# Optimization experiments

Hardware: AMD Instinct MI355X
Metric: run time of the kernel (lower is better)

The kernel has to match this reference:

```python
import jax, jax.numpy as jnp
import numpy as np

K = 5            # Chebyshev order (hard-coded in ManEmbedder conv_kwargs)
LAMBDA_MAX = 3.0 # fixed lambda_max from init
N_NODES = 100000
N_EDGES = 400000
N_GRAPHS = 64
H1, H2 = 128, 512


def _seg_sum(vals, idx, n):
    return jax.ops.segment_sum(vals, idx, num_segments=n)


def _cheb_edge_weights(edge_index, n_nodes):
    """Scaled Laplacian L_hat = 2*(I - D^-1/2 A D^-1/2)/lambda_max - I as edge weights.
    Matches PyG get_laplacian('sym') + ChebConv.__norm__ with fixed lambda_max.
    Degrees are computed at row = edge_index[0] (as in get_laplacian)."""
    row, col = edge_index[0], edge_index[1]
    ones = jnp.ones(row.shape[0], jnp.float32)
    deg = _seg_sum(ones, row, n_nodes)
    dinv = jnp.where(deg > 0, jax.lax.rsqrt(jnp.maximum(deg, 1e-12)), 0.0)
    w_edge = -(dinv[row] * dinv[col]) * (2.0 / LAMBDA_MAX)  # off-diagonal of L_hat
    w_loop = 2.0 / LAMBDA_MAX - 1.0                          # diagonal of L_hat (scalar)
    return w_edge, w_loop


def cheb_conv(x, edge_index, W, b, reverse):
    """PyG ChebConv. flow='target_to_source' (reverse=False): aggregate at row, gather at col.
    reverse=True flips the propagation direction (source_to_target)."""
    n = x.shape[0]
    w_edge, w_loop = _cheb_edge_weights(edge_index, n)
    row, col = edge_index[0], edge_index[1]
    src, dst = (row, col) if reverse else (col, row)

    def prop(h):  # L_hat @ h via gather-scale-scatter + diagonal term
        return _seg_sum(w_edge[:, None] * h[src], dst, n) + w_loop * h

    tx0 = x
    out = tx0 @ W[0]
    tx1 = prop(tx0)
    out = out + tx1 @ W[1]
    for k in range(2, K):
        tx2 = 2.0 * prop(tx1) - tx0
        out = out + tx2 @ W[k]
        tx0, tx1 = tx1, tx2
    return out + b


def bidir_block(x, edge_index, Wf, bf, Wb, bb):
    # Bidirectional: one ChebConv per edge direction, outputs summed.
    return cheb_conv(x, edge_index, Wf, bf, False) + cheb_conv(x, edge_index, Wb, bb, True)


def setup_inputs() -> dict:
    key = jax.random.key(0)
    ks = jax.random.split(key, 12)
    x = jax.random.normal(ks[0], (N_NODES, 1), jnp.float32)
    edge_index = jax.random.randint(ks[1], (2, N_EDGES), 0, N_NODES, dtype=jnp.int64)
    batch = jnp.sort(jax.random.randint(ks[2], (N_NODES,), 0, N_GRAPHS, dtype=jnp.int64))

    def glorot(k, shape):
        fan_in, fan_out = shape[-2], shape[-1]
        s = (6.0 / (fan_in + fan_out)) ** 0.5
        return jax.random.uniform(k, shape, jnp.float32, -s, s)

    return {
        "x": x, "edge_index": edge_index, "batch": batch,
        "W1f": glorot(ks[3], (K, 1, H1)),  "b1f": jnp.zeros((H1,), jnp.float32),
        "W1b": glorot(ks[4], (K, 1, H1)),  "b1b": jnp.zeros((H1,), jnp.float32),
        "W2f": glorot(ks[5], (K, H1, H2)), "b2f": jnp.zeros((H2,), jnp.float32),
        "W2b": glorot(ks[6], (K, H1, H2)), "b2b": jnp.zeros((H2,), jnp.float32),
    }


def reference(x, edge_index, batch, W1f, b1f, W1b, b1b, W2f, b2f, W2b, b2b):
    h = jax.nn.relu(bidir_block(x, edge_index, W1f, b1f, W1b, b1b))
    h = jax.nn.relu(bidir_block(h, edge_index, W2f, b2f, W2b, b2b))
    # global mean pool over batch index -> [N_GRAPHS, 512]
    summed = _seg_sum(h, batch, N_GRAPHS)
    counts = _seg_sum(jnp.ones((h.shape[0],), jnp.float32), batch, N_GRAPHS)
    return summed / jnp.maximum(counts, 1.0)[:, None]
```

## Files before the change

kernel.cpp:

```cpp
#include <hip/hip_runtime.h>
#include <hip/hip_bf16.h>

typedef unsigned short u16;
typedef unsigned int u32;
typedef __attribute__((ext_vector_type(4))) float f32x4;
typedef __attribute__((ext_vector_type(8))) short bf16x8;

struct __align__(8) ew_t { int s; float w; };

#define WLOOP (2.0f/3.0f - 1.0f)
#define WEDGE (-(2.0f/3.0f))

__device__ __forceinline__ float bf2f(u16 h){ u32 u = ((u32)h)<<16; float f; __builtin_memcpy(&f,&u,4); return f; }
__device__ __forceinline__ u16 f2bf(float f){ u32 u; __builtin_memcpy(&u,&f,4); u32 r = u + 0x7fffu + ((u>>16)&1u); return (u16)(r>>16); }

__device__ __forceinline__ void async16(u16* lds, const u16* g){
  __builtin_amdgcn_global_load_lds((const __attribute__((address_space(1))) u32*)g,
                                   (__attribute__((address_space(3))) u32*)lds, 16, 0, 0);
}

__global__ void k_hist(const int* __restrict__ ei, int E, int* cntf, int* cntb){
  int e = blockIdx.x*256 + threadIdx.x; if (e>=E) return;
  atomicAdd(&cntf[ei[e]],1); atomicAdd(&cntb[ei[E+e]],1);
}
__global__ void k_dinv(const int* __restrict__ cntf, float* dinv, int N){
  int n = blockIdx.x*256+threadIdx.x; if(n>=N) return;
  int d = cntf[n]; dinv[n] = d>0 ? rsqrtf((float)d) : 0.f;
}
__global__ void k_scanA(const int* __restrict__ cnt, int* excl, int* bsum, int n){
  __shared__ int sh[256]; int i = blockIdx.x*256+threadIdx.x;
  int v = (i<n)? cnt[i]:0; sh[threadIdx.x]=v; __syncthreads();
  for (int off=1; off<256; off<<=1){
    int t = (threadIdx.x>=off)? sh[threadIdx.x-off]:0; __syncthreads();
    sh[threadIdx.x]+=t; __syncthreads();
  }
  if (i<n) excl[i]=sh[threadIdx.x]-v;
  if (threadIdx.x==255) bsum[blockIdx.x]=sh[255];
}
__global__ void k_scanB(int* bsum, int nb, int* total){
  __shared__ int sh[512]; int t = threadIdx.x;
  int v = (t<nb)? bsum[t]:0; sh[t]=v; __syncthreads();
  for(int off=1; off<512; off<<=1){
    int a = (t>=off)? sh[t-off]:0; __syncthreads();
    sh[t]+=a; __syncthreads();
  }
  if (t<nb) bsum[t]=sh[t]-v;
  if (t==511) *total = sh[511];
}
__global__ void k_scanC(int* excl, const int* __restrict__ bsum, int n, int* cur){
  int i = blockIdx.x*256+threadIdx.x; if(i>=n) return;
  int v = excl[i]+bsum[blockIdx.x]; excl[i]=v; cur[i]=v;
}
__global__ void k_fill(const int* __restrict__ ei, int E, const float* __restrict__ dinv,
                       int* curf, int* curb, ew_t* ewf, ew_t* ewb){
  int e = blockIdx.x*256+threadIdx.x; if(e>=E) return;
  int r = ei[e], c = ei[E+e];
  float w = WEDGE * dinv[r]*dinv[c];
  int pf = atomicAdd(&curf[r],1); ewf[pf] = {c, w};
  int pb = atomicAdd(&curb[c],1); ewb[pb] = {r, w};
}

__global__ void k_sprop(const float* __restrict__ t1f, const float* __restrict__ t0f, float* df,
                        const float* __restrict__ t1b, const float* __restrict__ t0b, float* db,
                        const int* __restrict__ offf, const ew_t* __restrict__ ewfa,
                        const int* __restrict__ offb, const ew_t* __restrict__ ewba,
                        int N){
  int i = blockIdx.x*256+threadIdx.x;
  int dir = 0; if (i >= N){ i -= N; dir = 1; }
  if (i >= N) return;
  const float* t1; const float* t0; float* d; const int* off; const ew_t* ew;
  if (dir==0){ t1=t1f; t0=t0f; d=df; off=offf; ew=ewfa; }
  else       { t1=t1b; t0=t0b; d=db; off=offb; ew=ewba; }
  float a = WLOOP * t1[i];
  int e = off[i], e1 = off[i+1];
  for (; e+4<=e1; e+=4){
    ew_t p0=ew[e], p1=ew[e+1], p2=ew[e+2], p3=ew[e+3];
    float v0=t1[p0.s], v1=t1[p1.s], v2=t1[p2.s], v3=t1[p3.s];
    a += p0.w*v0 + p1.w*v1 + p2.w*v2 + p3.w*v3;
  }
  for (; e<e1; ++e){ ew_t p=ew[e]; a += p.w*t1[p.s]; }
  d[i] = t0 ? (2.f*a - t0[i]) : a;
}

__global__ void k_expand(const float* __restrict__ x,
   const float* __restrict__ cf1, const float* __restrict__ cf2, const float* __restrict__ cf3, const float* __restrict__ cf4,
   const float* __restrict__ cb1, const float* __restrict__ cb2, const float* __restrict__ cb3, const float* __restrict__ cb4,
   const float* __restrict__ W1f, const float* __restrict__ b1f,
   const float* __restrict__ W1b, const float* __restrict__ b1b,
   u16* __restrict__ T, int N){
  __shared__ float swf[640], swb[640], sbias[128];
  int tid = threadIdx.x;
  for (int i=tid;i<640;i+=256){ swf[i]=W1f[i]; swb[i]=W1b[i]; }
  if (tid<128) sbias[tid]=b1f[tid]+b1b[tid];
  __syncthreads();
  int j = tid & 127; int n = blockIdx.x*2 + (tid>>7);
  if (n>=N) return;
  float xx = x[n];
  float acc = sbias[j] + xx*(swf[j]+swb[j]);
  acc += cf1[n]*swf[128+j]; acc += cf2[n]*swf[256+j]; acc += cf3[n]*swf[384+j]; acc += cf4[n]*swf[512+j];
  acc += cb1[n]*swb[128+j]; acc += cb2[n]*swb[256+j]; acc += cb3[n]*swb[384+j]; acc += cb4[n]*swb[512+j];
  T[(size_t)n*1152 + j] = f2bf(fmaxf(acc,0.f));
}

__global__ void k_vprop(u16* __restrict__ T,
   const int* __restrict__ offf, const ew_t* __restrict__ ewfa,
   const int* __restrict__ offb, const ew_t* __restrict__ ewba,
   int ssf, int dsf, int psf, int ssb, int dsb, int psb, int N){
  int gid = blockIdx.x*256 + threadIdx.x;
  int l = threadIdx.x & 63, li = l & 15;
  int nd = (gid>>6)*4 + (l>>4);
  int dir = 0; if (nd >= N){ nd -= N; dir = 1; }
  bool alive = nd < N;
  int wid = alive ? nd : 0;
  const int* off; const ew_t* ew; int ss,ds,ps;
  if (!dir){ off=offf;ew=ewfa;ss=ssf;ds=dsf;ps=psf; }
  else     { off=offb;ew=ewba;ss=ssb;ds=dsb;ps=psb; }

  const u16* Trow = T + (size_t)ss*128 + li*8;
  bf16x8 sv = *(const bf16x8*)(Trow + (size_t)wid*1152);
  float a[8];
  #pragma unroll
  for (int q=0;q<8;q++) a[q] = WLOOP * bf2f((u16)sv[q]);

  int e0 = alive ? off[wid]   : 0;
  int e1 = alive ? off[wid+1] : 0;
  int deg = e1 - e0;
  int dm = max(deg, __shfl_xor(deg, 16));
  dm = max(dm, __shfl_xor(dm, 32));

  for (int j=0; j<dm; j+=2){
    bool a0v = j   < deg;
    bool a1v = j+1 < deg;
    ew_t p0 = ew[e0 + (a0v ? j   : 0)];
    ew_t p1 = ew[e0 + (a1v ? j+1 : 0)];
    float w0 = a0v ? p0.w : 0.f;
    float w1 = a1v ? p1.w : 0.f;
    int s0 = a0v ? p0.s : wid;
    int s1 = a1v ? p1.s : wid;
    bf16x8 n0 = *(const bf16x8*)(Trow + (size_t)s0*1152);
    bf16x8 n1 = *(const bf16x8*)(Trow + (size_t)s1*1152);
    #pragma unroll
    for (int q=0;q<8;q++) a[q] += w0*bf2f((u16)n0[q]) + w1*bf2f((u16)n1[q]);
  }

  float r[8];
  if (ps >= 0){
    bf16x8 pv = *(const bf16x8*)(T + (size_t)wid*1152 + (size_t)ps*128 + li*8);
    #pragma unroll
    for (int q=0;q<8;q++) r[q] = 2.f*a[q] - bf2f((u16)pv[q]);
  } else {
    #pragma unroll
    for (int q=0;q<8;q++) r[q] = a[q];
  }
  if (alive){
    bf16x8 o;
    #pragma unroll
    for (int q=0;q<8;q++) o[q] = (short)f2bf(r[q]);
    *(bf16x8*)(T + (size_t)wid*1152 + (size_t)ds*128 + li*8) = o;
  }
}

__global__ void k_wprep(const float* __restrict__ W2f, const float* __restrict__ W2b,
                        const float* __restrict__ b2f, const float* __restrict__ b2b,
                        u16* __restrict__ Wt2, float* __restrict__ bias2){
  int i = blockIdx.x*256+threadIdx.x;
  if (i < 512) bias2[i] = b2f[i]+b2b[i];
  if (i >= 512*1152) return;
  int j = i&7, l = (i>>3)&63, nt = (i>>9)&31, t = i>>14;
  int col = nt*16 + (l&15);
  int k   = t*32 + (l>>4)*8 + j;
  int s2 = k>>7, c = k&127;
  float v;
  if (s2==0)      v = W2f[c*512+col] + W2b[c*512+col];
  else if (s2<5)  v = W2f[(s2*128+c)*512 + col];
  else            v = W2b[((s2-4)*128+c)*512 + col];
  Wt2[i] = f2bf(v);
}

__global__ __launch_bounds__(256, 4) void k_gemm(const u16* __restrict__ T, const u16* __restrict__ Wt2,
                        const float* __restrict__ bias2, const int* __restrict__ batch,
                        float* __restrict__ outp, int Mvalid, int NB){
  int bid = blockIdx.x;
  int r8 = bid & 7, q = bid >> 3;
  int bn = q & 1, bm = (q >> 1)*8 + r8;
  if (bm >= NB) return;
  __shared__ u16 Al[2][64*32];
  int tid = threadIdx.x, w = tid>>6, l = tid&63;
  int wc = w;
  int hi = l>>4, lo = l&15;

  f32x4 acc[4][4];
  #pragma unroll
  for (int m=0;m<4;m++)
    #pragma unroll
    for (int n=0;n<4;n++){ acc[m][n][0]=0.f; acc[m][n][1]=0.f; acc[m][n][2]=0.f; acc[m][n][3]=0.f; }

  int sr = tid>>2, sp = tid&3;
  int csrc = ((sp ^ ((sr>>1)&3)))*8;
  const u16* asrc = T + (size_t)(bm*64 + sr)*1152 + csrc;
  const int adst = tid*8;
  int rsw = (hi ^ ((lo>>1)&3))*8;
  const int abase = lo*32 + rsw;
  const u16* bsrc = Wt2 + ((size_t)(bn*16 + wc*4)*64 + l)*8;

  #define LOADB(dst, t_) do { \
    _Pragma("unroll") \
    for (int n_=0;n_<4;n_++) dst[n_] = *(const bf16x8*)(bsrc + (size_t)(t_)*16384 + n_*512); \
  } while(0)

  bf16x8 be[4], bo[4];
  async16(&Al[0][adst], asrc);
  LOADB(be, 0);

  for (int t=0; t<36; t+=2){
    if (t < 35){
      async16(&Al[1][adst], asrc + (t+1)*32);
      LOADB(bo, t+1);
      asm volatile("s_waitcnt vmcnt(5)" ::: "memory");
    } else {
      asm volatile("s_waitcnt vmcnt(0)" ::: "memory");
    }
    asm volatile("s_barrier" ::: "memory");
    __builtin_amdgcn_s_setprio(1);
    #pragma unroll
    for (int m=0;m<4;m++){
      bf16x8 af = *(const bf16x8*)&Al[0][abase + m*512];
      #pragma unroll
      for (int n=0;n<4;n++)
        acc[m][n] = __builtin_amdgcn_mfma_f32_16x16x32_bf16(af, be[n], acc[m][n], 0, 0, 0);
    }
    __builtin_amdgcn_s_setprio(0);
    asm volatile("s_barrier" ::: "memory");
    if (t+2 < 36){
      async16(&Al[0][adst], asrc + (t+2)*32);
      LOADB(be, t+2);
      asm volatile("s_waitcnt vmcnt(5)" ::: "memory");
    } else {
      asm volatile("s_waitcnt vmcnt(0)" ::: "memory");
    }
    asm volatile("s_barrier" ::: "memory");
    __builtin_amdgcn_s_setprio(1);
    #pragma unroll
    for (int m=0;m<4;m++){
      bf16x8 af = *(const bf16x8*)&Al[1][abase + m*512];
      #pragma unroll
      for (int n=0;n<4;n++)
        acc[m][n] = __builtin_amdgcn_mfma_f32_16x16x32_bf16(af, bo[n], acc[m][n], 0, 0, 0);
    }
    __builtin_amdgcn_s_setprio(0);
    asm volatile("s_barrier" ::: "memory");
  }
  #undef LOADB

  int bg[16];
  #pragma unroll
  for (int m=0;m<4;m++)
    #pragma unroll
    for (int j2=0;j2<4;j2++){
      int row = bm*64 + m*16 + hi*4 + j2;
      bg[m*4+j2] = (row < Mvalid) ? batch[row] : -1;
    }
  #pragma unroll
  for (int n=0;n<4;n++){
    int col = bn*256 + wc*64 + n*16 + lo;
    float bc = bias2[col];
    int cg2 = -1; float ssum = 0.f;
    #pragma unroll
    for (int idx=0; idx<16; idx++){
      int g = bg[idx];
      if (g >= 0){
        float val = fmaxf(acc[idx>>2][n][idx&3] + bc, 0.f);
        if (g != cg2){ if (cg2 >= 0) atomicAdd(&outp[(cg2<<9) + col], ssum); cg2 = g; ssum = 0.f; }
        ssum += val;
      }
    }
    if (cg2 >= 0) atomicAdd(&outp[(cg2<<9) + col], ssum);
  }
}

__global__ void k_count(const int* __restrict__ batch, int* cg, int N){
  __shared__ int sh[64];
  int t = threadIdx.x;
  if (t < 64) sh[t] = 0;
  __syncthreads();
  int base = blockIdx.x*1024;
  #pragma unroll
  for (int i = base + t; i < base + 1024; i += 256){
    if (i < N) atomicAdd(&sh[batch[i]], 1);
  }
  __syncthreads();
  if (t < 64){ int v = sh[t]; if (v) atomicAdd(&cg[t], v); }
}

__global__ void k_div(float* out, const int* __restrict__ cg, int total){
  int i = blockIdx.x*256+threadIdx.x; if (i>=total) return;
  int g = i>>9; out[i] /= fmaxf((float)cg[g], 1.f);
}

extern "C" void kernel_launch(void* const* d_in, const int* in_sizes, int n_in,
                              void* d_out, int out_size, void* d_ws, size_t ws_size,
                              hipStream_t stream) {
  const float* x   = (const float*)d_in[0];
  const int*   ei  = (const int*)d_in[1];
  const int*   bat = (const int*)d_in[2];
  const float* W1f = (const float*)d_in[3];
  const float* b1f = (const float*)d_in[4];
  const float* W1b = (const float*)d_in[5];
  const float* b1b = (const float*)d_in[6];
  const float* W2f = (const float*)d_in[7];
  const float* b2f = (const float*)d_in[8];
  const float* W2b = (const float*)d_in[9];
  const float* b2b = (const float*)d_in[10];

  const int N  = in_sizes[0];
  const int E  = in_sizes[1] / 2;
  const int NP = ((N + 127)/128)*128;
  const int NB = ((N + 63)/64);

  size_t p = 0;
  auto A = [&](size_t sz){ size_t r = p; p += (sz + 255) & ~(size_t)255; return r; };
  size_t o_cnt  = A(2*(size_t)N*4);
  size_t o_offf = A(((size_t)N+1)*4);
  size_t o_offb = A(((size_t)N+1)*4);
  size_t o_curf = A((size_t)N*4);
  size_t o_curb = A((size_t)N*4);
  size_t o_bsum = A(512*4);
  size_t o_dinv = A((size_t)N*4);
  size_t o_ewf  = A((size_t)E*8);
  size_t o_ewb  = A((size_t)E*8);
  size_t o_cf   = A(8*(size_t)N*4);
  size_t o_Wt   = A((size_t)512*1152*2);
  size_t o_b2   = A(512*4);
  size_t o_cg   = A(64*4);
  size_t o_T    = A((size_t)NP*1152*2);
  if (p > ws_size) return;

  char* ws = (char*)d_ws;
  int*   cnt_f = (int*)(ws + o_cnt);
  int*   cnt_b = cnt_f + N;
  int*   off_f = (int*)(ws + o_offf);
  int*   off_b = (int*)(ws + o_offb);
  int*   cur_f = (int*)(ws + o_curf);
  int*   cur_b = (int*)(ws + o_curb);
  int*   bsum  = (int*)(ws + o_bsum);
  float* dinv  = (float*)(ws + o_dinv);
  ew_t*  ewf   = (ew_t*)(ws + o_ewf);
  ew_t*  ewb   = (ew_t*)(ws + o_ewb);
  float* cf1   = (float*)(ws + o_cf);
  float* cf2   = cf1 + N; float* cf3 = cf2 + N; float* cf4 = cf3 + N;
  float* cb1   = cf4 + N; float* cb2 = cb1 + N; float* cb3 = cb2 + N; float* cb4 = cb3 + N;
  u16*   Wt2   = (u16*)(ws + o_Wt);
  float* bias2 = (float*)(ws + o_b2);
  int*   cg    = (int*)(ws + o_cg);
  u16*   T     = (u16*)(ws + o_T);
  float* outp  = (float*)d_out;

  const int nbN = (N + 255)/256;
  const int nbE = (E + 255)/256;
  const int nb2N = (2*N + 255)/256;

  hipMemsetAsync(cnt_f, 0, 2*(size_t)N*4, stream);
  hipMemsetAsync(cg, 0, 64*4, stream);
  hipMemsetAsync(d_out, 0, (size_t)out_size*4, stream);
  if (NP > N) hipMemsetAsync(T + (size_t)N*1152, 0, (size_t)(NP-N)*1152*2, stream);

  k_hist<<<nbE,256,0,stream>>>(ei, E, cnt_f, cnt_b);
  k_dinv<<<nbN,256,0,stream>>>(cnt_f, dinv, N);
  k_scanA<<<nbN,256,0,stream>>>(cnt_f, off_f, bsum, N);
  k_scanB<<<1,512,0,stream>>>(bsum, nbN, off_f + N);
  k_scanC<<<nbN,256,0,stream>>>(off_f, bsum, N, cur_f);
  k_scanA<<<nbN,256,0,stream>>>(cnt_b, off_b, bsum, N);
  k_scanB<<<1,512,0,stream>>>(bsum, nbN, off_b + N);
  k_scanC<<<nbN,256,0,stream>>>(off_b, bsum, N, cur_b);
  k_fill<<<nbE,256,0,stream>>>(ei, E, dinv, cur_f, cur_b, ewf, ewb);

  k_sprop<<<nb2N,256,0,stream>>>(x,   nullptr, cf1,  x,   nullptr, cb1, off_f,ewf, off_b,ewb, N);
  k_sprop<<<nb2N,256,0,stream>>>(cf1, x,       cf2,  cb1, x,       cb2, off_f,ewf, off_b,ewb, N);
  k_sprop<<<nb2N,256,0,stream>>>(cf2, cf1,     cf3,  cb2, cb1,     cb3, off_f,ewf, off_b,ewb, N);
  k_sprop<<<nb2N,256,0,stream>>>(cf3, cf2,     cf4,  cb3, cb2,     cb4, off_f,ewf, off_b,ewb, N);
  k_expand<<<(N+1)/2,256,0,stream>>>(x, cf1,cf2,cf3,cf4, cb1,cb2,cb3,cb4, W1f,b1f,W1b,b1b, T, N);

  k_wprep<<<(512*1152+255)/256,256,0,stream>>>(W2f, W2b, b2f, b2b, Wt2, bias2);

  const int vb = (2*N*16 + 255)/256;
  k_vprop<<<vb,256,0,stream>>>(T, off_f,ewf, off_b,ewb, 0,1,-1, 0,5,-1, N);
  k_vprop<<<vb,256,0,stream>>>(T, off_f,ewf, off_b,ewb, 1,2, 0, 5,6, 0, N);
  k_vprop<<<vb,256,0,stream>>>(T, off_f,ewf, off_b,ewb, 2,3, 1, 6,7, 5, N);
  k_vprop<<<vb,256,0,stream>>>(T, off_f,ewf, off_b,ewb, 3,4, 2, 7,8, 6, N);

  k_count<<<(N+1023)/1024,256,0,stream>>>(bat, cg, N);
  const int gemmGrid = ((NB + 7)/8)*8*2;
  k_gemm<<<gemmGrid,256,0,stream>>>(T, Wt2, bias2, bat, outp, N, NB);
  k_div<<<(out_size+255)/256,256,0,stream>>>(outp, cg, out_size);
}
```

Before: 524.7 us.

## Switch GEMM to single-wave blocks to drop LDS barriers

Restructures the bf16 MFMA GEMM so each block is one wave computing a 64x64 tile, with the wave staging its own A tile into LDS. This removes the workgroup barriers around every k-step and raises the block count fourfold. In exchange, A tiles are no longer shared across four waves, so the T matrix is read from global memory four times more often.

```diff
diff --git a/kernel.cpp b/kernel.cpp
--- a/kernel.cpp
+++ b/kernel.cpp
@@ -177,16 +177,15 @@
   Wt2[i] = f2bf(v);
 }
 
-__global__ __launch_bounds__(256, 4) void k_gemm(const u16* __restrict__ T, const u16* __restrict__ Wt2,
+__global__ __launch_bounds__(64, 4) void k_gemm(const u16* __restrict__ T, const u16* __restrict__ Wt2,
                         const float* __restrict__ bias2, const int* __restrict__ batch,
                         float* __restrict__ outp, int Mvalid, int NB){
   int bid = blockIdx.x;
   int r8 = bid & 7, q = bid >> 3;
-  int bn = q & 1, bm = (q >> 1)*8 + r8;
+  int bn = q & 7, bm = (q >> 3)*8 + r8;
   if (bm >= NB) return;
-  __shared__ u16 Al[2][64*32];
-  int tid = threadIdx.x, w = tid>>6, l = tid&63;
-  int wc = w;
+  __shared__ u16 Al[2][2048];
+  int l = threadIdx.x;
   int hi = l>>4, lo = l&15;
 
   f32x4 acc[4][4];
@@ -195,32 +194,42 @@
     #pragma unroll
     for (int n=0;n<4;n++){ acc[m][n][0]=0.f; acc[m][n][1]=0.f; acc[m][n][2]=0.f; acc[m][n][3]=0.f; }
 
-  int sr = tid>>2, sp = tid&3;
-  int csrc = ((sp ^ ((sr>>1)&3)))*8;
-  const u16* asrc = T + (size_t)(bm*64 + sr)*1152 + csrc;
-  const int adst = tid*8;
+  const u16* asrc0; const u16* asrc1; const u16* asrc2; const u16* asrc3;
+  {
+    int sp = l&3;
+    int sr0 = 0*16 + (l>>2), sr1 = 1*16 + (l>>2), sr2 = 2*16 + (l>>2), sr3 = 3*16 + (l>>2);
+    asrc0 = T + (size_t)(bm*64 + sr0)*1152 + (sp ^ ((sr0>>1)&3))*8;
+    asrc1 = T + (size_t)(bm*64 + sr1)*1152 + (sp ^ ((sr1>>1)&3))*8;
+    asrc2 = T + (size_t)(bm*64 + sr2)*1152 + (sp ^ ((sr2>>1)&3))*8;
+    asrc3 = T + (size_t)(bm*64 + sr3)*1152 + (sp ^ ((sr3>>1)&3))*8;
+  }
   int rsw = (hi ^ ((lo>>1)&3))*8;
   const int abase = lo*32 + rsw;
-  const u16* bsrc = Wt2 + ((size_t)(bn*16 + wc*4)*64 + l)*8;
-
+  const u16* bsrc = Wt2 + ((size_t)(bn*4)*64 + l)*8;
+
+  #define STAGEA(buf, kk) do { \
+    async16(&Al[buf][0*512 + l*8], asrc0 + (kk)); \
+    async16(&Al[buf][1*512 + l*8], asrc1 + (kk)); \
+    async16(&Al[buf][2*512 + l*8], asrc2 + (kk)); \
+    async16(&Al[buf][3*512 + l*8], asrc3 + (kk)); \
+  } while(0)
   #define LOADB(dst, t_) do { \
     _Pragma("unroll") \
     for (int n_=0;n_<4;n_++) dst[n_] = *(const bf16x8*)(bsrc + (size_t)(t_)*16384 + n_*512); \
   } while(0)
 
   bf16x8 be[4], bo[4];
-  async16(&Al[0][adst], asrc);
+  STAGEA(0, 0);
   LOADB(be, 0);
 
   for (int t=0; t<36; t+=2){
     if (t < 35){
-      async16(&Al[1][adst], asrc + (t+1)*32);
+      STAGEA(1, (t+1)*32);
       LOADB(bo, t+1);
-      asm volatile("s_waitcnt vmcnt(5)" ::: "memory");
+      asm volatile("s_waitcnt vmcnt(8)" ::: "memory");
     } else {
       asm volatile("s_waitcnt vmcnt(0)" ::: "memory");
     }
-    asm volatile("s_barrier" ::: "memory");
     __builtin_amdgcn_s_setprio(1);
     #pragma unroll
     for (int m=0;m<4;m++){
@@ -230,15 +239,13 @@
         acc[m][n] = __builtin_amdgcn_mfma_f32_16x16x32_bf16(af, be[n], acc[m][n], 0, 0, 0);
     }
     __builtin_amdgcn_s_setprio(0);
-    asm volatile("s_barrier" ::: "memory");
     if (t+2 < 36){
-      async16(&Al[0][adst], asrc + (t+2)*32);
+      STAGEA(0, (t+2)*32);
       LOADB(be, t+2);
-      asm volatile("s_waitcnt vmcnt(5)" ::: "memory");
+      asm volatile("s_waitcnt vmcnt(8)" ::: "memory");
     } else {
       asm volatile("s_waitcnt vmcnt(0)" ::: "memory");
     }
-    asm volatile("s_barrier" ::: "memory");
     __builtin_amdgcn_s_setprio(1);
     #pragma unroll
     for (int m=0;m<4;m++){
@@ -248,8 +255,8 @@
         acc[m][n] = __builtin_amdgcn_mfma_f32_16x16x32_bf16(af, bo[n], acc[m][n], 0, 0, 0);
     }
     __builtin_amdgcn_s_setprio(0);
-    asm volatile("s_barrier" ::: "memory");
-  }
+  }
+  #undef STAGEA
   #undef LOADB
 
   int bg[16];
@@ -262,7 +269,7 @@
     }
   #pragma unroll
   for (int n=0;n<4;n++){
-    int col = bn*256 + wc*64 + n*16 + lo;
+    int col = bn*64 + n*16 + lo;
     float bc = bias2[col];
     int cg2 = -1; float ssum = 0.f;
     #pragma unroll
@@ -389,7 +396,7 @@
   k_vprop<<<vb,256,0,stream>>>(T, off_f,ewf, off_b,ewb, 3,4, 2, 7,8, 6, N);
 
   k_count<<<(N+1023)/1024,256,0,stream>>>(bat, cg, N);
-  const int gemmGrid = ((NB + 7)/8)*8*2;
-  k_gemm<<<gemmGrid,256,0,stream>>>(T, Wt2, bias2, bat, outp, N, NB);
+  const int gemmGrid = ((NB + 7)/8)*8*8;
+  k_gemm<<<gemmGrid,64,0,stream>>>(T, Wt2, bias2, bat, outp, N, NB);
   k_div<<<(out_size+255)/256,256,0,stream>>>(outp, cg, out_size);
 }
```

Result: slower. 603.7 us (+15.1%).

## Sort nodes by degree so propagation wavefronts get balanced edge loops

Applied to the files above, without the earlier changes.

Adds a degree histogram, scan and scatter that build a per-direction node permutation ordered by in-degree (capped at 63). The scalar and vector propagation kernels then process nodes in that permuted order, so lanes in a wavefront have similar degrees and less divergence in the edge loop. In exchange, node reads and writes become scattered instead of coalesced, and three small kernels plus an extra indirection load are added.

```diff
diff --git a/kernel.cpp b/kernel.cpp
--- a/kernel.cpp
+++ b/kernel.cpp
@@ -60,26 +60,53 @@
   int pb = atomicAdd(&curb[c],1); ewb[pb] = {r, w};
 }
 
+__global__ void k_dhist(const int* __restrict__ cf, const int* __restrict__ cb, int* dh, int N){
+  __shared__ int sh[128];
+  int t = threadIdx.x; if (t<128) sh[t]=0; __syncthreads();
+  int n = blockIdx.x*256 + t;
+  if (n<N){ atomicAdd(&sh[min(cf[n],63)],1); atomicAdd(&sh[64+min(cb[n],63)],1); }
+  __syncthreads();
+  if (t<128){ int v=sh[t]; if(v) atomicAdd(&dh[t],v); }
+}
+__global__ void k_dscan(int* dh){
+  __shared__ int sh[128]; int t = threadIdx.x;
+  int v = dh[t]; sh[t]=v; __syncthreads();
+  int base = t & 64;
+  for (int off=1; off<64; off<<=1){
+    int a = (t-off >= base)? sh[t-off] : 0; __syncthreads();
+    sh[t] += a; __syncthreads();
+  }
+  dh[t] = sh[t] - v;
+}
+__global__ void k_dscatter(const int* __restrict__ cf, const int* __restrict__ cb,
+                           int* dh, int* permf, int* permb, int N){
+  int n = blockIdx.x*256+threadIdx.x; if(n>=N) return;
+  int pf = atomicAdd(&dh[min(cf[n],63)],1);     permf[pf]=n;
+  int pb = atomicAdd(&dh[64+min(cb[n],63)],1);  permb[pb]=n;
+}
+
 __global__ void k_sprop(const float* __restrict__ t1f, const float* __restrict__ t0f, float* df,
                         const float* __restrict__ t1b, const float* __restrict__ t0b, float* db,
                         const int* __restrict__ offf, const ew_t* __restrict__ ewfa,
                         const int* __restrict__ offb, const ew_t* __restrict__ ewba,
+                        const int* __restrict__ permf, const int* __restrict__ permb,
                         int N){
   int i = blockIdx.x*256+threadIdx.x;
   int dir = 0; if (i >= N){ i -= N; dir = 1; }
   if (i >= N) return;
-  const float* t1; const float* t0; float* d; const int* off; const ew_t* ew;
-  if (dir==0){ t1=t1f; t0=t0f; d=df; off=offf; ew=ewfa; }
-  else       { t1=t1b; t0=t0b; d=db; off=offb; ew=ewba; }
-  float a = WLOOP * t1[i];
-  int e = off[i], e1 = off[i+1];
+  const float* t1; const float* t0; float* d; const int* off; const ew_t* ew; const int* pm;
+  if (dir==0){ t1=t1f; t0=t0f; d=df; off=offf; ew=ewfa; pm=permf; }
+  else       { t1=t1b; t0=t0b; d=db; off=offb; ew=ewba; pm=permb; }
+  int node = pm[i];
+  float a = WLOOP * t1[node];
+  int e = off[node], e1 = off[node+1];
   for (; e+4<=e1; e+=4){
     ew_t p0=ew[e], p1=ew[e+1], p2=ew[e+2], p3=ew[e+3];
     float v0=t1[p0.s], v1=t1[p1.s], v2=t1[p2.s], v3=t1[p3.s];
     a += p0.w*v0 + p1.w*v1 + p2.w*v2 + p3.w*v3;
   }
   for (; e<e1; ++e){ ew_t p=ew[e]; a += p.w*t1[p.s]; }
-  d[i] = t0 ? (2.f*a - t0[i]) : a;
+  d[node] = t0 ? (2.f*a - t0[node]) : a;
 }
 
 __global__ void k_expand(const float* __restrict__ x,
@@ -105,16 +132,17 @@
 __global__ void k_vprop(u16* __restrict__ T,
    const int* __restrict__ offf, const ew_t* __restrict__ ewfa,
    const int* __restrict__ offb, const ew_t* __restrict__ ewba,
+   const int* __restrict__ permf, const int* __restrict__ permb,
    int ssf, int dsf, int psf, int ssb, int dsb, int psb, int N){
   int gid = blockIdx.x*256 + threadIdx.x;
   int l = threadIdx.x & 63, li = l & 15;
   int nd = (gid>>6)*4 + (l>>4);
   int dir = 0; if (nd >= N){ nd -= N; dir = 1; }
   bool alive = nd < N;
-  int wid = alive ? nd : 0;
-  const int* off; const ew_t* ew; int ss,ds,ps;
-  if (!dir){ off=offf;ew=ewfa;ss=ssf;ds=dsf;ps=psf; }
-  else     { off=offb;ew=ewba;ss=ssb;ds=dsb;ps=psb; }
+  const int* off; const ew_t* ew; const int* pm; int ss,ds,ps;
+  if (!dir){ off=offf;ew=ewfa;pm=permf;ss=ssf;ds=dsf;ps=psf; }
+  else     { off=offb;ew=ewba;pm=permb;ss=ssb;ds=dsb;ps=psb; }
+  int wid = alive ? pm[nd] : 0;
 
   const u16* Trow = T + (size_t)ss*128 + li*8;
   bf16x8 sv = *(const bf16x8*)(Trow + (size_t)wid*1152);
@@ -332,6 +360,8 @@
   size_t o_Wt   = A((size_t)512*1152*2);
   size_t o_b2   = A(512*4);
   size_t o_cg   = A(64*4);
+  size_t o_dh   = A(128*4);
+  size_t o_perm = A(2*(size_t)N*4);
   size_t o_T    = A((size_t)NP*1152*2);
   if (p > ws_size) return;
 
@@ -352,6 +382,9 @@
   u16*   Wt2   = (u16*)(ws + o_Wt);
   float* bias2 = (float*)(ws + o_b2);
   int*   cg    = (int*)(ws + o_cg);
+  int*   dh    = (int*)(ws + o_dh);
+  int*   permf = (int*)(ws + o_perm);
+  int*   permb = permf + N;
   u16*   T     = (u16*)(ws + o_T);
   float* outp  = (float*)d_out;
 
@@ -361,6 +394,7 @@
 
   hipMemsetAsync(cnt_f, 0, 2*(size_t)N*4, stream);
   hipMemsetAsync(cg, 0, 64*4, stream);
+  hipMemsetAsync(dh, 0, 128*4, stream);
   hipMemsetAsync(d_out, 0, (size_t)out_size*4, stream);
   if (NP > N) hipMemsetAsync(T + (size_t)N*1152, 0, (size_t)(NP-N)*1152*2, stream);
 
@@ -374,19 +408,23 @@
   k_scanC<<<nbN,256,0,stream>>>(off_b, bsum, N, cur_b);
   k_fill<<<nbE,256,0,stream>>>(ei, E, dinv, cur_f, cur_b, ewf, ewb);
 
-  k_sprop<<<nb2N,256,0,stream>>>(x,   nullptr, cf1,  x,   nullptr, cb1, off_f,ewf, off_b,ewb, N);
-  k_sprop<<<nb2N,256,0,stream>>>(cf1, x,       cf2,  cb1, x,       cb2, off_f,ewf, off_b,ewb, N);
-  k_sprop<<<nb2N,256,0,stream>>>(cf2, cf1,     cf3,  cb2, cb1,     cb3, off_f,ewf, off_b,ewb, N);
-  k_sprop<<<nb2N,256,0,stream>>>(cf3, cf2,     cf4,  cb3, cb2,     cb4, off_f,ewf, off_b,ewb, N);
+  k_dhist<<<nbN,256,0,stream>>>(cnt_f, cnt_b, dh, N);
+  k_dscan<<<1,128,0,stream>>>(dh);
+  k_dscatter<<<nbN,256,0,stream>>>(cnt_f, cnt_b, dh, permf, permb, N);
+
+  k_sprop<<<nb2N,256,0,stream>>>(x,   nullptr, cf1,  x,   nullptr, cb1, off_f,ewf, off_b,ewb, permf,permb, N);
+  k_sprop<<<nb2N,256,0,stream>>>(cf1, x,       cf2,  cb1, x,       cb2, off_f,ewf, off_b,ewb, permf,permb, N);
+  k_sprop<<<nb2N,256,0,stream>>>(cf2, cf1,     cf3,  cb2, cb1,     cb3, off_f,ewf, off_b,ewb, permf,permb, N);
+  k_sprop<<<nb2N,256,0,stream>>>(cf3, cf2,     cf4,  cb3, cb2,     cb4, off_f,ewf, off_b,ewb, permf,permb, N);
   k_expand<<<(N+1)/2,256,0,stream>>>(x, cf1,cf2,cf3,cf4, cb1,cb2,cb3,cb4, W1f,b1f,W1b,b1b, T, N);
 
   k_wprep<<<(512*1152+255)/256,256,0,stream>>>(W2f, W2b, b2f, b2b, Wt2, bias2);
 
   const int vb = (2*N*16 + 255)/256;
-  k_vprop<<<vb,256,0,stream>>>(T, off_f,ewf, off_b,ewb, 0,1,-1, 0,5,-1, N);
-  k_vprop<<<vb,256,0,stream>>>(T, off_f,ewf, off_b,ewb, 1,2, 0, 5,6, 0, N);
-  k_vprop<<<vb,256,0,stream>>>(T, off_f,ewf, off_b,ewb, 2,3, 1, 6,7, 5, N);
-  k_vprop<<<vb,256,0,stream>>>(T, off_f,ewf, off_b,ewb, 3,4, 2, 7,8, 6, N);
+  k_vprop<<<vb,256,0,stream>>>(T, off_f,ewf, off_b,ewb, permf,permb, 0,1,-1, 0,5,-1, N);
+  k_vprop<<<vb,256,0,stream>>>(T, off_f,ewf, off_b,ewb, permf,permb, 1,2, 0, 5,6, 0, N);
+  k_vprop<<<vb,256,0,stream>>>(T, off_f,ewf, off_b,ewb, permf,permb, 2,3, 1, 6,7, 5, N);
+  k_vprop<<<vb,256,0,stream>>>(T, off_f,ewf, off_b,ewb, permf,permb, 3,4, 2, 7,8, 6, N);
 
   k_count<<<(N+1023)/1024,256,0,stream>>>(bat, cg, N);
   const int gemmGrid = ((NB + 7)/8)*8*2;
```

After: 1.260 ms. 2.4x slower.
